# Kernel tuning notes

Measured on AMD Instinct MI355X. Metric: run time of the kernel, lower is better.

## Reference

```python
import jax, jax.numpy as jnp
import numpy as np

N, M, D, E, NLAYER = 200000, 100000, 64, 1000000, 3
EPS = 0.1
TLEN = (24, 7)


def l2norm(x):
    # F.normalize(dim=-1) with eps=1e-12 clamp on the norm
    n = jnp.linalg.norm(x, axis=-1, keepdims=True)
    return x / jnp.maximum(n, 1e-12)


def setup_inputs() -> dict:
    key = jax.random.key(0)
    ks = jax.random.split(key, 8)
    u_id = jax.random.randint(ks[0], (E,), 0, N)
    i_id = jax.random.randint(ks[1], (E,), 0, M)
    T = jnp.stack([
        jax.random.randint(ks[2], (E,), 0, TLEN[0]),
        jax.random.randint(ks[3], (E,), 0, TLEN[1]),
    ], axis=1)
    # xavier-uniform-ish init for embedding tables
    lim_u = np.sqrt(6.0 / (N + D)).astype(np.float32)
    lim_i = np.sqrt(6.0 / (M + D)).astype(np.float32)
    user_emb = jax.random.uniform(ks[4], (N, D), minval=-lim_u, maxval=lim_u)
    item_emb = jax.random.uniform(ks[5], (M, D), minval=-lim_i, maxval=lim_i)
    # xavier-normal time tables, each [tlen_i, D//tdim]
    W0 = jax.random.normal(ks[6], (TLEN[0], D // 2)) * np.sqrt(2.0 / (TLEN[0] + D // 2))
    W1 = jax.random.normal(ks[7], (TLEN[1], D // 2)) * np.sqrt(2.0 / (TLEN[1] + D // 2))
    beta = jnp.float32(0.3)
    return {"u_id": u_id, "i_id": i_id, "T": T, "beta": beta,
            "user_emb": user_emb, "item_emb": item_emb, "W0": W0, "W1": W1}


def _forward(u_id, i_id, T, beta, user_emb, item_emb, W0, W1):
    # TimeEncoder: one_hot(t) @ W == W[t]; concat over time dims -> [E, D]
    t_emb = jnp.concatenate([W0[T[:, 0]], W1[T[:, 1]]], axis=-1)
    u_t = l2norm(user_emb[u_id] + t_emb)
    i_t = l2norm(item_emb[i_id] + t_emb)
    s = ((u_t * i_t).sum(axis=-1) + 1.0) * 0.5      # cosine sim mapped to [0,1]
    s = jnp.where(s < beta, 0.0, s)                  # threshold

    # coalesced sparse COO mm: duplicates are summed by segment_sum anyway
    def spmm_u(X):  # A_r @ X : [n, d]
        return jax.ops.segment_sum(s[:, None] * X[i_id], u_id, num_segments=N)

    def spmm_i(X):  # A_r.T @ X : [m, d]
        return jax.ops.segment_sum(s[:, None] * X[u_id], i_id, num_segments=M)

    # pass 1: clean propagation
    u_embs, i_embs = [user_emb], [item_emb]
    for _ in range(NLAYER):
        u_embs.append(spmm_u(i_embs[-1]))
        i_embs.append(spmm_i(u_embs[-2]))
    u_fwd = jnp.mean(jnp.stack(u_embs[1:], 0), 0)
    i_fwd = jnp.mean(jnp.stack(i_embs[1:], 0), 0)

    # passes 2 & 3: perturbed propagation with randperm-row noise
    def perturbed_pass(base_key):
        u_embs, i_embs = [user_emb], [item_emb]
        for l in range(NLAYER):
            ku, ki = jax.random.split(jax.random.fold_in(base_key, l))
            u_emb = spmm_u(i_embs[-1])
            i_emb = spmm_i(u_embs[-1])
            u_emb = u_emb + l2norm(u_emb[jax.random.permutation(ku, N)]) * EPS
            i_emb = i_emb + l2norm(i_emb[jax.random.permutation(ki, M)]) * EPS
            u_embs.append(u_emb)
            i_embs.append(i_emb)
        return (jnp.mean(jnp.stack(u_embs[1:], 0), 0),
                jnp.mean(jnp.stack(i_embs[1:], 0), 0))

    u_p1, i_p1 = perturbed_pass(jax.random.key(1))
    u_p2, i_p2 = perturbed_pass(jax.random.key(2))
    return u_fwd, i_fwd, u_p1, i_p1, u_p2, i_p2


def reference(u_id, i_id, T, beta, user_emb, item_emb, W0, W1):
    return _forward(u_id, i_id, T, beta, user_emb, item_emb, W0, W1)
```

## Files before the change

### kernel.cpp

```cpp
#include <hip/hip_runtime.h>
#include <stdint.h>

#define NU 200000
#define NI 100000
#define DD 64
#define NE 1000000
#define EPSV 0.1f
#define NBUCK 65536
#define NSORT 12
#define PAIR (NU + NI)
#define TOTSORT (6 * PAIR)
#define NBALL (NSORT * NBUCK)
#define SCAN_TPB 256
#define SCAN_ELEMS 1024
#define CEILDIV(a,b) (((a)+(b)-1)/(b))

__host__ __device__ inline void tf2x32(uint32_t k0, uint32_t k1,
                                       uint32_t x0, uint32_t x1,
                                       uint32_t &o0, uint32_t &o1) {
  uint32_t ks0 = k0, ks1 = k1, ks2 = k0 ^ k1 ^ 0x1BD11BDAu;
  x0 += ks0; x1 += ks1;
#define TF_RND(r) { x0 += x1; x1 = (x1 << (r)) | (x1 >> (32 - (r))); x1 ^= x0; }
  TF_RND(13) TF_RND(15) TF_RND(26) TF_RND(6)   x0 += ks1; x1 += ks2 + 1u;
  TF_RND(17) TF_RND(29) TF_RND(16) TF_RND(24)  x0 += ks2; x1 += ks0 + 2u;
  TF_RND(13) TF_RND(15) TF_RND(26) TF_RND(6)   x0 += ks0; x1 += ks1 + 3u;
  TF_RND(17) TF_RND(29) TF_RND(16) TF_RND(24)  x0 += ks1; x1 += ks2 + 4u;
  TF_RND(13) TF_RND(15) TF_RND(26) TF_RND(6)   x0 += ks2; x1 += ks0 + 5u;
#undef TF_RND
  o0 = x0; o1 = x1;
}

struct K2 { uint32_t a, b; };
static inline K2 h_tf(K2 k, uint32_t x0, uint32_t x1) {
  K2 r; tf2x32(k.a, k.b, x0, x1, r.a, r.b); return r;
}

struct SortKeys { uint32_t a[NSORT]; uint32_t b[NSORT]; };

__device__ inline void regionOf(int gid, int &r, int &local) {
  int pairIdx = gid / PAIR;
  int rem = gid - pairIdx * PAIR;
  if (rem < NU) { r = pairIdx * 2;     local = rem; }
  else          { r = pairIdx * 2 + 1; local = rem - NU; }
}

__global__ void k_edgesc(const int* __restrict__ u_id, const int* __restrict__ i_id,
                         const int* __restrict__ T, const float* __restrict__ betap,
                         const float* __restrict__ UE, const float* __restrict__ IE,
                         const float* __restrict__ W0, const float* __restrict__ W1,
                         int* __restrict__ cur_u, int* __restrict__ cur_i,
                         uint2* __restrict__ colw_u, uint2* __restrict__ colw_i)
{
  int g = blockIdx.x * blockDim.x + threadIdx.x;
  int e = g >> 4, lane = g & 15;
  if (e >= NE) return;
  int u = u_id[e], it = i_id[e];
  float4 a = ((const float4*)UE)[u * 16 + lane];
  float4 b = ((const float4*)IE)[it * 16 + lane];
  float4 t;
  if (lane < 8) t = ((const float4*)W0)[T[2 * e] * 8 + lane];
  else          t = ((const float4*)W1)[T[2 * e + 1] * 8 + (lane - 8)];
  float ux = a.x + t.x, uy = a.y + t.y, uz = a.z + t.z, uw = a.w + t.w;
  float ix = b.x + t.x, iy = b.y + t.y, iz = b.z + t.z, iw = b.w + t.w;
  float uu = ux * ux + uy * uy + uz * uz + uw * uw;
  float ii = ix * ix + iy * iy + iz * iz + iw * iw;
  float ui = ux * ix + uy * iy + uz * iz + uw * iw;
#pragma unroll
  for (int m = 1; m < 16; m <<= 1) {
    uu += __shfl_xor(uu, m);
    ii += __shfl_xor(ii, m);
    ui += __shfl_xor(ui, m);
  }
  if (lane == 0) {
    float c = ui / (fmaxf(sqrtf(uu), 1e-12f) * fmaxf(sqrtf(ii), 1e-12f));
    float sv = (c + 1.0f) * 0.5f;
    float w = (sv < betap[0]) ? 0.0f : sv;
    uint32_t wb = __float_as_uint(w);
    int pu = atomicAdd(&cur_u[u], 1);
    colw_u[pu] = make_uint2((uint32_t)it, wb);
    int pi = atomicAdd(&cur_i[it], 1);
    colw_i[pi] = make_uint2((uint32_t)u, wb);
  }
}

__global__ void k_scan1(const int* __restrict__ in, int n, int* __restrict__ partials)
{
  __shared__ int sdata[SCAN_TPB];
  int base = blockIdx.x * SCAN_ELEMS;
  int sum = 0;
  for (int j = threadIdx.x; j < SCAN_ELEMS; j += SCAN_TPB) {
    int idx = base + j;
    if (idx < n) sum += in[idx];
  }
  sdata[threadIdx.x] = sum;
  __syncthreads();
  for (int off = SCAN_TPB / 2; off > 0; off >>= 1) {
    if (threadIdx.x < off) sdata[threadIdx.x] += sdata[threadIdx.x + off];
    __syncthreads();
  }
  if (threadIdx.x == 0) partials[blockIdx.x] = sdata[0];
}

__global__ void k_scan2(int* __restrict__ partials, int nb, int* __restrict__ endPtr)
{
  __shared__ int part[1024];
  int tid = threadIdx.x;
  part[tid] = (tid < nb) ? partials[tid] : 0;
  __syncthreads();
  for (int off = 1; off < 1024; off <<= 1) {
    int t = (tid >= off) ? part[tid - off] : 0;
    __syncthreads();
    part[tid] += t;
    __syncthreads();
  }
  if (tid < nb) partials[tid] = tid ? part[tid - 1] : 0;
  if (tid == 1023 && endPtr) *endPtr = part[1023];
}

__global__ void k_scan3(const int* __restrict__ in, int n,
                        const int* __restrict__ partials,
                        int* __restrict__ offs, int* __restrict__ cursor)
{
  __shared__ int sdata[SCAN_TPB];
  int base = blockIdx.x * SCAN_ELEMS + threadIdx.x * 4;
  int v[4];
#pragma unroll
  for (int q = 0; q < 4; ++q) v[q] = (base + q < n) ? in[base + q] : 0;
  int tsum = v[0] + v[1] + v[2] + v[3];
  sdata[threadIdx.x] = tsum;
  __syncthreads();
  for (int off = 1; off < SCAN_TPB; off <<= 1) {
    int t = (threadIdx.x >= off) ? sdata[threadIdx.x - off] : 0;
    __syncthreads();
    sdata[threadIdx.x] += t;
    __syncthreads();
  }
  int excl = partials[blockIdx.x] + (threadIdx.x ? sdata[threadIdx.x - 1] : 0);
#pragma unroll
  for (int q = 0; q < 4; ++q) {
    if (base + q < n) {
      offs[base + q] = excl;
      if (cursor) cursor[base + q] = excl;
      excl += v[q];
    }
  }
}

static void scan_ex(hipStream_t st, const int* in, int n, int* offs, int* cursor,
                    int* partials, int* endPtr)
{
  int nb = CEILDIV(n, SCAN_ELEMS);
  k_scan1<<<nb, SCAN_TPB, 0, st>>>(in, n, partials);
  k_scan2<<<1, 1024, 0, st>>>(partials, nb, endPtr);
  k_scan3<<<nb, SCAN_TPB, 0, st>>>(in, n, partials, offs, cursor);
}

__global__ void k_count(const int* __restrict__ u_id, const int* __restrict__ i_id,
                        int* __restrict__ cnt_u, int* __restrict__ cnt_i)
{
  int e = blockIdx.x * blockDim.x + threadIdx.x;
  if (e < NE) {
    atomicAdd(&cnt_u[u_id[e]], 1);
    atomicAdd(&cnt_i[i_id[e]], 1);
  }
}

__global__ void k_spmm2(const int* __restrict__ ptr_u, const uint2* __restrict__ colw_u,
                        const float* __restrict__ Xi_in,
                        const int* __restrict__ ptr_i, const uint2* __restrict__ colw_i,
                        const float* __restrict__ Xu_in,
                        float* __restrict__ Y, float* __restrict__ acc,
                        int first, float scale, int writeY)
{
  int g = blockIdx.x * blockDim.x + threadIdx.x;
  int r = g >> 4, lane = g & 15;
  if (r >= PAIR) return;
  const int* ptr; const uint2* colw; const float4* X; int rr;
  if (r < NU) { ptr = ptr_u; colw = colw_u; X = (const float4*)Xi_in; rr = r; }
  else        { ptr = ptr_i; colw = colw_i; X = (const float4*)Xu_in; rr = r - NU; }
  int b = ptr[rr], e2 = ptr[rr + 1];
  float4 a = make_float4(0.f, 0.f, 0.f, 0.f);
  for (int k = b; k < e2; ++k) {
    uint2 cw = colw[k];
    float wk = __uint_as_float(cw.y);
    float4 x = X[(size_t)cw.x * 16 + lane];
    a.x += wk * x.x; a.y += wk * x.y; a.z += wk * x.z; a.w += wk * x.w;
  }
  if (writeY) ((float4*)Y)[r * 16 + lane] = a;
  if (acc) {
    float4 v;
    if (first) v = a;
    else {
      v = ((const float4*)acc)[r * 16 + lane];
      v.x += a.x; v.y += a.y; v.z += a.z; v.w += a.w;
    }
    v.x *= scale; v.y *= scale; v.z *= scale; v.w *= scale;
    ((float4*)acc)[r * 16 + lane] = v;
  }
}

__global__ void k_noise2(const float* __restrict__ S, const int* __restrict__ perm,
                         float* __restrict__ O, float* __restrict__ acc,
                         int first, float scale, int writeO)
{
  int g = blockIdx.x * blockDim.x + threadIdx.x;
  int r = g >> 4, lane = g & 15;
  if (r >= PAIR) return;
  int pr = (r < NU) ? perm[r] : NU + perm[r];
  float4 z = ((const float4*)S)[(size_t)pr * 16 + lane];
  float ss = z.x * z.x + z.y * z.y + z.z * z.z + z.w * z.w;
#pragma unroll
  for (int m = 1; m < 16; m <<= 1) ss += __shfl_xor(ss, m);
  float coef = EPSV / fmaxf(sqrtf(ss), 1e-12f);
  float4 v = ((const float4*)S)[(size_t)r * 16 + lane];
  v.x += coef * z.x; v.y += coef * z.y; v.z += coef * z.z; v.w += coef * z.w;
  if (writeO) ((float4*)O)[r * 16 + lane] = v;
  float4 a;
  if (first) a = v;
  else {
    a = ((const float4*)acc)[r * 16 + lane];
    a.x += v.x; a.y += v.y; a.z += v.z; a.w += v.w;
  }
  a.x *= scale; a.y *= scale; a.z *= scale; a.w *= scale;
  ((float4*)acc)[r * 16 + lane] = a;
}

__global__ void k_genkeys_all(SortKeys sk, uint32_t* __restrict__ keys)
{
  int gid = blockIdx.x * blockDim.x + threadIdx.x;
  if (gid >= TOTSORT) return;
  int r, local; regionOf(gid, r, local);
  uint32_t o0, o1;
  tf2x32(sk.a[r], sk.b[r], 0u, (uint32_t)local, o0, o1);
  keys[gid] = o0 ^ o1;
}

__global__ void k_hist_all(const uint32_t* __restrict__ keys, int* __restrict__ hist)
{
  int gid = blockIdx.x * blockDim.x + threadIdx.x;
  if (gid >= TOTSORT) return;
  int r, local; regionOf(gid, r, local);
  atomicAdd(&hist[r * NBUCK + (keys[gid] >> 16)], 1);
}

__global__ void k_scatter_all(const uint32_t* __restrict__ keys,
                              const int* __restrict__ valsIn,
                              int* __restrict__ cursor,
                              uint32_t* __restrict__ keyO, int* __restrict__ valO,
                              int* __restrict__ posO)
{
  int gid = blockIdx.x * blockDim.x + threadIdx.x;
  if (gid >= TOTSORT) return;
  int r, local; regionOf(gid, r, local);
  uint32_t k = keys[gid];
  int p = atomicAdd(&cursor[r * NBUCK + (k >> 16)], 1);
  keyO[p] = k;
  valO[p] = valsIn ? valsIn[gid] : local;
  posO[p] = local;
}

__global__ void k_fixup(const int* __restrict__ offs, uint32_t* __restrict__ keyO,
                        int* __restrict__ valO, int* __restrict__ posO)
{
  int b = blockIdx.x * blockDim.x + threadIdx.x;
  if (b >= NBALL) return;
  int s0 = offs[b], e0 = offs[b + 1];
  for (int i = s0 + 1; i < e0; ++i) {
    uint32_t k = keyO[i]; int v = valO[i], p = posO[i];
    int j = i - 1;
    while (j >= s0 && (keyO[j] > k || (keyO[j] == k && posO[j] > p))) {
      keyO[j + 1] = keyO[j]; valO[j + 1] = valO[j]; posO[j + 1] = posO[j];
      --j;
    }
    keyO[j + 1] = k; valO[j + 1] = v; posO[j + 1] = p;
  }
}

extern "C" void kernel_launch(void* const* d_in, const int* in_sizes, int n_in,
                              void* d_out, int out_size, void* d_ws, size_t ws_size,
                              hipStream_t stream)
{
  const int*   u_id = (const int*)d_in[0];
  const int*   i_id = (const int*)d_in[1];
  const int*   T    = (const int*)d_in[2];
  const float* beta = (const float*)d_in[3];
  const float* UE   = (const float*)d_in[4];
  const float* IE   = (const float*)d_in[5];
  const float* W0   = (const float*)d_in[6];
  const float* W1   = (const float*)d_in[7];
  (void)in_sizes; (void)n_in; (void)out_size;

  float* out    = (float*)d_out;
  float* accCln = out;
  float* accP0  = out + (size_t)PAIR * DD;
  float* accP1  = out + 2ull * PAIR * DD;

  char* wp = (char*)d_ws;
  auto carve = [&](size_t bytes) -> char* {
    char* r = wp; wp += (bytes + 255) & ~(size_t)255; return r;
  };
  int*   ptr_u    = (int*)  carve(4ull * (NU + 1));
  int*   cnt_u    = (int*)  carve(4ull * NU);
  int*   cur_u    = (int*)  carve(4ull * NU);
  int*   ptr_i    = (int*)  carve(4ull * (NI + 1));
  int*   cnt_i    = (int*)  carve(4ull * NI);
  int*   cur_i    = (int*)  carve(4ull * NI);
  uint2* colw_u   = (uint2*)carve(8ull * NE);
  uint2* colw_i   = (uint2*)carve(8ull * NE);
  int*   perms    = (int*)  carve(4ull * TOTSORT);
  int*   partials = (int*)  carve(4ull * 1025);

  const size_t PB = (size_t)PAIR * DD * 4;
  size_t used = (size_t)(wp - (char*)d_ws);
  bool share = ws_size >= used + 3 * PB;
  char* uni = carve(share ? 3 * PB : 2 * PB);

  float* P0 = (float*)uni;
  float* P1 = P0 + (size_t)PAIR * DD;
  float* P2 = share ? P1 + (size_t)PAIR * DD : nullptr;

  uint32_t* keysA = (uint32_t*)uni;
  uint32_t* keyB  = keysA + TOTSORT;
  int*      posB  = (int*)(keyB + TOTSORT);
  int*      val0  = posB + TOTSORT;
  int*      hist  = val0 + TOTSORT;
  int*      offs  = hist + NBALL;
  int*      curs  = offs + NBALL + 1;

  hipMemsetAsync(cnt_u, 0, 4 * NU, stream);
  hipMemsetAsync(cnt_i, 0, 4 * NI, stream);
  k_count<<<CEILDIV(NE, 256), 256, 0, stream>>>(u_id, i_id, cnt_u, cnt_i);
  scan_ex(stream, cnt_u, NU, ptr_u, cur_u, partials, &ptr_u[NU]);
  scan_ex(stream, cnt_i, NI, ptr_i, cur_i, partials, &ptr_i[NI]);
  k_edgesc<<<CEILDIV(NE * 16, 256), 256, 0, stream>>>(u_id, i_id, T, beta, UE, IE,
                                                      W0, W1, cur_u, cur_i,
                                                      colw_u, colw_i);

  SortKeys sk0, sk1;
  for (int p = 0; p < 2; ++p) {
    K2 base = {0u, (uint32_t)(p + 1)};
    for (int l = 0; l < 3; ++l) {
      K2 kl = h_tf(base, 0u, (uint32_t)l);
      K2 kk[2] = { h_tf(kl, 0u, 0u), h_tf(kl, 0u, 1u) };
      for (int q = 0; q < 2; ++q) {
        int r = (p * 3 + l) * 2 + q;
        K2 kperm = kk[q];
        K2 knext = h_tf(kperm, 0u, 0u);
        K2 sub0  = h_tf(kperm, 0u, 1u);
        K2 sub1  = h_tf(knext, 0u, 1u);
        sk0.a[r] = sub0.a; sk0.b[r] = sub0.b;
        sk1.a[r] = sub1.a; sk1.b[r] = sub1.b;
      }
    }
  }
  const int GS = CEILDIV(TOTSORT, 256), GF = CEILDIV(NBALL, 256);
  k_genkeys_all<<<GS, 256, 0, stream>>>(sk0, keysA);
  hipMemsetAsync(hist, 0, 4ull * NBALL, stream);
  k_hist_all<<<GS, 256, 0, stream>>>(keysA, hist);
  scan_ex(stream, hist, NBALL, offs, curs, partials, &offs[NBALL]);
  k_scatter_all<<<GS, 256, 0, stream>>>(keysA, (const int*)nullptr, curs, keyB, val0, posB);
  k_fixup<<<GF, 256, 0, stream>>>(offs, keyB, val0, posB);
  k_genkeys_all<<<GS, 256, 0, stream>>>(sk1, keysA);
  hipMemsetAsync(hist, 0, 4ull * NBALL, stream);
  k_hist_all<<<GS, 256, 0, stream>>>(keysA, hist);
  scan_ex(stream, hist, NBALL, offs, curs, partials, &offs[NBALL]);
  k_scatter_all<<<GS, 256, 0, stream>>>(keysA, val0, curs, keyB, perms, posB);
  k_fixup<<<GF, 256, 0, stream>>>(offs, keyB, perms, posB);

  const int GP = CEILDIV(PAIR * 16, 256);
  const float THIRD = 1.0f / 3.0f;
  auto SPMM = [&](const float* Xi_in, const float* Xu_in, float* Y, float* acc,
                  int first, float scale, int writeY) {
    k_spmm2<<<GP, 256, 0, stream>>>(ptr_u, colw_u, Xi_in, ptr_i, colw_i, Xu_in,
                                    Y, acc, first, scale, writeY);
  };
  auto NOISE = [&](const float* S, int pass, int layer, float* O, float* acc,
                   int first, float scale, int writeO) {
    k_noise2<<<GP, 256, 0, stream>>>(S, perms + (size_t)(pass * 3 + layer) * PAIR,
                                     O, acc, first, scale, writeO);
  };

  if (share) {
    SPMM(IE, UE, P0, accCln, 1, 1.0f, 1);
    SPMM(P0 + (size_t)NU * DD, P0, P1, accCln, 0, 1.0f, 1);
    SPMM(P1 + (size_t)NU * DD, P1, nullptr, accCln, 0, THIRD, 0);
    for (int p = 0; p < 2; ++p) {
      float* acc = p ? accP1 : accP0;
      NOISE(P0, p, 0, P1, acc, 1, 1.0f, 1);
      SPMM(P1 + (size_t)NU * DD, P1, P2, nullptr, 0, 1.0f, 1);
      NOISE(P2, p, 1, P1, acc, 0, 1.0f, 1);
      SPMM(P1 + (size_t)NU * DD, P1, P2, nullptr, 0, 1.0f, 1);
      NOISE(P2, p, 2, nullptr, acc, 0, THIRD, 0);
    }
  } else {
    SPMM(IE, UE, P0, accCln, 1, 1.0f, 1);
    SPMM(P0 + (size_t)NU * DD, P0, P1, accCln, 0, 1.0f, 1);
    SPMM(P1 + (size_t)NU * DD, P1, nullptr, accCln, 0, THIRD, 0);
    for (int p = 0; p < 2; ++p) {
      float* acc = p ? accP1 : accP0;
      SPMM(IE, UE, P0, nullptr, 0, 1.0f, 1);
      NOISE(P0, p, 0, P1, acc, 1, 1.0f, 1);
      SPMM(P1 + (size_t)NU * DD, P1, P0, nullptr, 0, 1.0f, 1);
      NOISE(P0, p, 1, P1, acc, 0, 1.0f, 1);
      SPMM(P1 + (size_t)NU * DD, P1, P0, nullptr, 0, 1.0f, 1);
      NOISE(P0, p, 2, nullptr, acc, 0, THIRD, 0);
    }
  }
}
```

Before: 1.957 ms.

## Fuse key generation with histogram, unroll SpMM loop, reuse accumulators as layer buffers

Merges the key-generation and histogram kernels so the keys are not reread, and unrolls the SpMM edge loop by two so two gathers are in flight per iteration. The sort drops the separate val array and stores positions in posA instead. The propagation schedule always uses two scratch buffers: first-layer noisy outputs are written straight into the accumulators and used as SpMM input, which removes the extra SpMM recompute on the low-workspace path and the separate P2 buffer. This relies on the accumulator holding exactly the layer output after the first noise step (first=1, scale 1), and it reorders the layers across passes.

```diff
diff --git a/kernel.cpp b/kernel.cpp
--- a/kernel.cpp
+++ b/kernel.cpp
@@ -180,7 +180,17 @@
   else        { ptr = ptr_i; colw = colw_i; X = (const float4*)Xu_in; rr = r - NU; }
   int b = ptr[rr], e2 = ptr[rr + 1];
   float4 a = make_float4(0.f, 0.f, 0.f, 0.f);
-  for (int k = b; k < e2; ++k) {
+  int k = b;
+  for (; k + 1 < e2; k += 2) {
+    uint2 cw0 = colw[k];
+    uint2 cw1 = colw[k + 1];
+    float4 x0 = X[(size_t)cw0.x * 16 + lane];
+    float4 x1 = X[(size_t)cw1.x * 16 + lane];
+    float w0 = __uint_as_float(cw0.y), w1 = __uint_as_float(cw1.y);
+    a.x += w0 * x0.x; a.y += w0 * x0.y; a.z += w0 * x0.z; a.w += w0 * x0.w;
+    a.x += w1 * x1.x; a.y += w1 * x1.y; a.z += w1 * x1.z; a.w += w1 * x1.w;
+  }
+  if (k < e2) {
     uint2 cw = colw[k];
     float wk = __uint_as_float(cw.y);
     float4 x = X[(size_t)cw.x * 16 + lane];
@@ -225,22 +235,16 @@
   ((float4*)acc)[r * 16 + lane] = a;
 }
 
-__global__ void k_genkeys_all(SortKeys sk, uint32_t* __restrict__ keys)
+__global__ void k_genhist(SortKeys sk, uint32_t* __restrict__ keys, int* __restrict__ hist)
 {
   int gid = blockIdx.x * blockDim.x + threadIdx.x;
   if (gid >= TOTSORT) return;
   int r, local; regionOf(gid, r, local);
   uint32_t o0, o1;
   tf2x32(sk.a[r], sk.b[r], 0u, (uint32_t)local, o0, o1);
-  keys[gid] = o0 ^ o1;
-}
-
-__global__ void k_hist_all(const uint32_t* __restrict__ keys, int* __restrict__ hist)
-{
-  int gid = blockIdx.x * blockDim.x + threadIdx.x;
-  if (gid >= TOTSORT) return;
-  int r, local; regionOf(gid, r, local);
-  atomicAdd(&hist[r * NBUCK + (keys[gid] >> 16)], 1);
+  uint32_t kk = o0 ^ o1;
+  keys[gid] = kk;
+  atomicAdd(&hist[r * NBUCK + (kk >> 16)], 1);
 }
 
 __global__ void k_scatter_all(const uint32_t* __restrict__ keys,
@@ -255,7 +259,7 @@
   uint32_t k = keys[gid];
   int p = atomicAdd(&cursor[r * NBUCK + (k >> 16)], 1);
   keyO[p] = k;
-  valO[p] = valsIn ? valsIn[gid] : local;
+  if (valO) valO[p] = valsIn ? valsIn[gid] : local;
   posO[p] = local;
 }
 
@@ -266,13 +270,16 @@
   if (b >= NBALL) return;
   int s0 = offs[b], e0 = offs[b + 1];
   for (int i = s0 + 1; i < e0; ++i) {
-    uint32_t k = keyO[i]; int v = valO[i], p = posO[i];
+    uint32_t k = keyO[i]; int p = posO[i];
+    int v = valO ? valO[i] : 0;
     int j = i - 1;
     while (j >= s0 && (keyO[j] > k || (keyO[j] == k && posO[j] > p))) {
-      keyO[j + 1] = keyO[j]; valO[j + 1] = valO[j]; posO[j + 1] = posO[j];
+      keyO[j + 1] = keyO[j]; posO[j + 1] = posO[j];
+      if (valO) valO[j + 1] = valO[j];
       --j;
     }
-    keyO[j + 1] = k; valO[j + 1] = v; posO[j + 1] = p;
+    keyO[j + 1] = k; posO[j + 1] = p;
+    if (valO) valO[j + 1] = v;
   }
 }
 
@@ -288,7 +295,7 @@
   const float* IE   = (const float*)d_in[5];
   const float* W0   = (const float*)d_in[6];
   const float* W1   = (const float*)d_in[7];
-  (void)in_sizes; (void)n_in; (void)out_size;
+  (void)in_sizes; (void)n_in; (void)out_size; (void)ws_size;
 
   float* out    = (float*)d_out;
   float* accCln = out;
@@ -311,19 +318,16 @@
   int*   partials = (int*)  carve(4ull * 1025);
 
   const size_t PB = (size_t)PAIR * DD * 4;
-  size_t used = (size_t)(wp - (char*)d_ws);
-  bool share = ws_size >= used + 3 * PB;
-  char* uni = carve(share ? 3 * PB : 2 * PB);
+  char* uni = carve(2 * PB);
 
   float* P0 = (float*)uni;
   float* P1 = P0 + (size_t)PAIR * DD;
-  float* P2 = share ? P1 + (size_t)PAIR * DD : nullptr;
 
   uint32_t* keysA = (uint32_t*)uni;
   uint32_t* keyB  = keysA + TOTSORT;
-  int*      posB  = (int*)(keyB + TOTSORT);
-  int*      val0  = posB + TOTSORT;
-  int*      hist  = val0 + TOTSORT;
+  int*      posA  = (int*)(keyB + TOTSORT);
+  int*      posB  = posA + TOTSORT;
+  int*      hist  = posB + TOTSORT;
   int*      offs  = hist + NBALL;
   int*      curs  = offs + NBALL + 1;
 
@@ -354,25 +358,29 @@
     }
   }
   const int GS = CEILDIV(TOTSORT, 256), GF = CEILDIV(NBALL, 256);
-  k_genkeys_all<<<GS, 256, 0, stream>>>(sk0, keysA);
   hipMemsetAsync(hist, 0, 4ull * NBALL, stream);
-  k_hist_all<<<GS, 256, 0, stream>>>(keysA, hist);
+  k_genhist<<<GS, 256, 0, stream>>>(sk0, keysA, hist);
   scan_ex(stream, hist, NBALL, offs, curs, partials, &offs[NBALL]);
-  k_scatter_all<<<GS, 256, 0, stream>>>(keysA, (const int*)nullptr, curs, keyB, val0, posB);
-  k_fixup<<<GF, 256, 0, stream>>>(offs, keyB, val0, posB);
-  k_genkeys_all<<<GS, 256, 0, stream>>>(sk1, keysA);
+  k_scatter_all<<<GS, 256, 0, stream>>>(keysA, (const int*)nullptr, curs,
+                                        keyB, (int*)nullptr, posA);
+  k_fixup<<<GF, 256, 0, stream>>>(offs, keyB, (int*)nullptr, posA);
   hipMemsetAsync(hist, 0, 4ull * NBALL, stream);
-  k_hist_all<<<GS, 256, 0, stream>>>(keysA, hist);
+  k_genhist<<<GS, 256, 0, stream>>>(sk1, keysA, hist);
   scan_ex(stream, hist, NBALL, offs, curs, partials, &offs[NBALL]);
-  k_scatter_all<<<GS, 256, 0, stream>>>(keysA, val0, curs, keyB, perms, posB);
+  k_scatter_all<<<GS, 256, 0, stream>>>(keysA, posA, curs, keyB, perms, posB);
   k_fixup<<<GF, 256, 0, stream>>>(offs, keyB, perms, posB);
 
   const int GP = CEILDIV(PAIR * 16, 256);
   const float THIRD = 1.0f / 3.0f;
-  auto SPMM = [&](const float* Xi_in, const float* Xu_in, float* Y, float* acc,
+  auto SPMM = [&](const float* in, float* Y, float* acc,
                   int first, float scale, int writeY) {
-    k_spmm2<<<GP, 256, 0, stream>>>(ptr_u, colw_u, Xi_in, ptr_i, colw_i, Xu_in,
+    k_spmm2<<<GP, 256, 0, stream>>>(ptr_u, colw_u, in + (size_t)NU * DD,
+                                    ptr_i, colw_i, in,
                                     Y, acc, first, scale, writeY);
+  };
+  auto SPMM0 = [&]() {
+    k_spmm2<<<GP, 256, 0, stream>>>(ptr_u, colw_u, IE, ptr_i, colw_i, UE,
+                                    P0, accCln, 1, 1.0f, 1);
   };
   auto NOISE = [&](const float* S, int pass, int layer, float* O, float* acc,
                    int first, float scale, int writeO) {
@@ -380,30 +388,17 @@
                                      O, acc, first, scale, writeO);
   };
 
-  if (share) {
-    SPMM(IE, UE, P0, accCln, 1, 1.0f, 1);
-    SPMM(P0 + (size_t)NU * DD, P0, P1, accCln, 0, 1.0f, 1);
-    SPMM(P1 + (size_t)NU * DD, P1, nullptr, accCln, 0, THIRD, 0);
-    for (int p = 0; p < 2; ++p) {
-      float* acc = p ? accP1 : accP0;
-      NOISE(P0, p, 0, P1, acc, 1, 1.0f, 1);
-      SPMM(P1 + (size_t)NU * DD, P1, P2, nullptr, 0, 1.0f, 1);
-      NOISE(P2, p, 1, P1, acc, 0, 1.0f, 1);
-      SPMM(P1 + (size_t)NU * DD, P1, P2, nullptr, 0, 1.0f, 1);
-      NOISE(P2, p, 2, nullptr, acc, 0, THIRD, 0);
-    }
-  } else {
-    SPMM(IE, UE, P0, accCln, 1, 1.0f, 1);
-    SPMM(P0 + (size_t)NU * DD, P0, P1, accCln, 0, 1.0f, 1);
-    SPMM(P1 + (size_t)NU * DD, P1, nullptr, accCln, 0, THIRD, 0);
-    for (int p = 0; p < 2; ++p) {
-      float* acc = p ? accP1 : accP0;
-      SPMM(IE, UE, P0, nullptr, 0, 1.0f, 1);
-      NOISE(P0, p, 0, P1, acc, 1, 1.0f, 1);
-      SPMM(P1 + (size_t)NU * DD, P1, P0, nullptr, 0, 1.0f, 1);
-      NOISE(P0, p, 1, P1, acc, 0, 1.0f, 1);
-      SPMM(P1 + (size_t)NU * DD, P1, P0, nullptr, 0, 1.0f, 1);
-      NOISE(P0, p, 2, nullptr, acc, 0, THIRD, 0);
-    }
-  }
-}
+  SPMM0();
+  SPMM(P0, P1, accCln, 0, 1.0f, 1);
+  SPMM(P1, nullptr, accCln, 0, THIRD, 0);
+  NOISE(P0, 0, 0, nullptr, accP0, 1, 1.0f, 0);
+  NOISE(P0, 1, 0, nullptr, accP1, 1, 1.0f, 0);
+  SPMM(accP0, P1, nullptr, 0, 1.0f, 1);
+  NOISE(P1, 0, 1, P0, accP0, 0, 1.0f, 1);
+  SPMM(P0, P1, nullptr, 0, 1.0f, 1);
+  NOISE(P1, 0, 2, nullptr, accP0, 0, THIRD, 0);
+  SPMM(accP1, P1, nullptr, 0, 1.0f, 1);
+  NOISE(P1, 1, 1, P0, accP1, 0, 1.0f, 1);
+  SPMM(P0, P1, nullptr, 0, 1.0f, 1);
+  NOISE(P1, 1, 2, nullptr, accP1, 0, THIRD, 0);
+}
```

New measurement: 1.874 ms. 4.2% less time.
